# Optimization experiments

Measured on AMD Instinct MI355X. Metric: run time of the kernel, lower is better.

## Reference

```python
import jax, jax.numpy as jnp
import numpy as np

N = 100000   # nodes
F = 32       # input features
E = 1600000  # edges
G = 512      # graphs
EPS = 1e-5   # BatchNorm eps


def setup_inputs() -> dict:
    key = jax.random.key(0)
    ks = jax.random.split(key, 12)
    x = jax.random.normal(ks[0], (N, F), jnp.float32)
    edge_index = jax.random.randint(ks[1], (2, E), 0, N)
    batch = jnp.sort(jax.random.randint(ks[2], (N,), 0, G))

    def glorot(k, i, o):
        return jax.random.normal(k, (i, o), jnp.float32) * (1.0 / np.sqrt(i))

    return {
        "x": x, "edge_index": edge_index, "batch": batch,
        "W1": glorot(ks[3], F, 16), "b1": jnp.zeros((16,), jnp.float32),
        "g1": jnp.ones((16,), jnp.float32), "be1": jnp.zeros((16,), jnp.float32),
        "W2": glorot(ks[4], 16, 64), "b2": jnp.zeros((64,), jnp.float32),
        "g2": jnp.ones((64,), jnp.float32), "be2": jnp.zeros((64,), jnp.float32),
        "W3": glorot(ks[5], 64, 64), "b3": jnp.zeros((64,), jnp.float32),
        "Wc": glorot(ks[6], 64, 1), "bc": jnp.zeros((1,), jnp.float32),
    }


def _gcn_conv(h, src, dst, dis, W, b, n):
    # PyG GCNConv: D^{-1/2}(A+I)D^{-1/2} X W + b (self-loops folded in analytically)
    hw = h @ W                                   # [N, out]
    msg = hw[src] * (dis[src] * dis[dst])[:, None]   # gather + normalize, [E, out]
    agg = jax.ops.segment_sum(msg, dst, num_segments=n)  # scatter-add
    agg = agg + hw * (dis * dis)[:, None]        # self-loop contribution
    return agg + b


def _bn(h, g, b):
    # BatchNorm1d, training mode (biased variance over node axis)
    m = jnp.mean(h, axis=0)
    v = jnp.mean((h - m) ** 2, axis=0)
    return (h - m) * jax.lax.rsqrt(v + EPS) * g + b


def reference(x, edge_index, batch, W1, b1, g1, be1, W2, b2, g2, be2, W3, b3, Wc, bc):
    n = x.shape[0]
    src, dst = edge_index[0], edge_index[1]
    # degree including self-loops (computed on target nodes, edge weight 1)
    deg = jax.ops.segment_sum(jnp.ones((src.shape[0],), x.dtype), dst, num_segments=n) + 1.0
    dis = jax.lax.rsqrt(deg)

    h = jnp.tanh(_gcn_conv(x, src, dst, dis, W1, b1, n))
    h = _bn(h, g1, be1)
    h = jnp.tanh(_gcn_conv(h, src, dst, dis, W2, b2, n))
    h = _bn(h, g2, be2)
    h = jnp.tanh(_gcn_conv(h, src, dst, dis, W3, b3, n))

    # global_mean_pool over graph ids
    sums = jax.ops.segment_sum(h, batch, num_segments=G)          # [G, 64]
    cnts = jax.ops.segment_sum(jnp.ones((n,), x.dtype), batch, num_segments=G)
    pooled = sums / jnp.maximum(cnts, 1.0)[:, None]

    return pooled @ Wc + bc   # [G, 1]
```

## Files before the change

### kernel.cpp

```cpp
#include <hip/hip_runtime.h>

#define EPSV 1e-5f
#define EB 512
#define NPB 256
#define NBUK_MAX 512

typedef __attribute__((ext_vector_type(8))) short bf16x8;
typedef __attribute__((ext_vector_type(4))) float f32x4;
typedef unsigned short ushort_t;

__device__ inline unsigned f2bf(float f){
  unsigned u = __float_as_uint(f);
  u += 0x7fffu + ((u>>16)&1u);
  return u>>16;
}
#define BF_LO(u) __uint_as_float((u)<<16)
#define BF_HI(u) __uint_as_float((u)&0xffff0000u)

__global__ __launch_bounds__(256) void k_csr_count(const int* __restrict__ dst, int E, int chunk,
                                                   int nbuk, int* __restrict__ cnt){
  __shared__ int hist[NBUK_MAX];
  int t = threadIdx.x, b = blockIdx.x;
  for(int k=t; k<nbuk; k+=256) hist[k]=0;
  __syncthreads();
  int lo = b*chunk, hi = lo+chunk < E ? lo+chunk : E;
  for(int i=lo+t*4; i+3<hi; i+=1024){
    int4 d4 = *(const int4*)(dst + i);
    atomicAdd(&hist[d4.x>>8], 1); atomicAdd(&hist[d4.y>>8], 1);
    atomicAdd(&hist[d4.z>>8], 1); atomicAdd(&hist[d4.w>>8], 1);
  }
  int rem = lo + ((hi - lo) & ~3);
  for(int i=rem+t; i<hi; i+=256) atomicAdd(&hist[dst[i]>>8], 1);
  __syncthreads();
  for(int k=t; k<nbuk; k+=256) cnt[(size_t)k*EB + b] = hist[k];
}

__global__ __launch_bounds__(1024) void k_scan_local(const int* __restrict__ v_in, int L,
                                                     int* __restrict__ loc, int* __restrict__ blk){
  __shared__ int ps[1024];
  int t = threadIdx.x;
  int i = blockIdx.x*1024 + t;
  int v = (i < L) ? v_in[i] : 0;
  ps[t] = v;
  __syncthreads();
  for(int off=1; off<1024; off<<=1){
    int u = (t>=off) ? ps[t-off] : 0;
    __syncthreads();
    ps[t] += u;
    __syncthreads();
  }
  if(i < L) loc[i] = ps[t] - v;
  if(t == 1023) blk[blockIdx.x] = ps[t];
}

__global__ __launch_bounds__(1024) void k_scan_sums(int* __restrict__ blk, int nb,
                                                    int* __restrict__ totalOut){
  __shared__ int ps[1024];
  int t = threadIdx.x;
  int v = (t < nb) ? blk[t] : 0;
  ps[t] = v;
  __syncthreads();
  for(int off=1; off<1024; off<<=1){
    int u = (t>=off) ? ps[t-off] : 0;
    __syncthreads();
    ps[t] += u;
    __syncthreads();
  }
  if(t < nb) blk[t] = ps[t] - v;
  if(t == 1023) *totalOut = ps[t];
}

__global__ __launch_bounds__(256) void k_csr_scatter(const int* __restrict__ src,
                                                     const int* __restrict__ dst,
                                                     const int* __restrict__ loc,
                                                     const int* __restrict__ blk,
                                                     int E, int chunk, int nbuk,
                                                     unsigned* __restrict__ epk){
  __shared__ int cur[NBUK_MAX];
  int t = threadIdx.x, b = blockIdx.x;
  for(int k=t; k<nbuk; k+=256){
    int i = k*EB + b;
    cur[k] = loc[i] + blk[i>>10];
  }
  __syncthreads();
  int lo = b*chunk, hi = lo+chunk < E ? lo+chunk : E;
  for(int i=lo+t*4; i+3<hi; i+=1024){
    int4 s4 = *(const int4*)(src + i);
    int4 d4 = *(const int4*)(dst + i);
    int p0 = atomicAdd(&cur[d4.x>>8], 1);
    epk[p0] = ((unsigned)s4.x<<8) | (unsigned)(d4.x & 255);
    int p1 = atomicAdd(&cur[d4.y>>8], 1);
    epk[p1] = ((unsigned)s4.y<<8) | (unsigned)(d4.y & 255);
    int p2 = atomicAdd(&cur[d4.z>>8], 1);
    epk[p2] = ((unsigned)s4.z<<8) | (unsigned)(d4.z & 255);
    int p3 = atomicAdd(&cur[d4.w>>8], 1);
    epk[p3] = ((unsigned)s4.w<<8) | (unsigned)(d4.w & 255);
  }
  int rem = lo + ((hi - lo) & ~3);
  for(int i=rem+t; i<hi; i+=256){
    int d = dst[i];
    int p = atomicAdd(&cur[d>>8], 1);
    epk[p] = ((unsigned)src[i]<<8) | (unsigned)(d & 255);
  }
}

__global__ __launch_bounds__(256) void k_csr_final(const unsigned* __restrict__ epk,
                                                   const int* __restrict__ loc,
                                                   const int* __restrict__ blk,
                                                   int nbuk, int N, int E,
                                                   int* __restrict__ rp, float* __restrict__ dis,
                                                   int* __restrict__ csr_src){
  __shared__ int hist[NPB], ps[NPB], cur[NPB];
  int t = threadIdx.x, k = blockIdx.x;
  int i0 = k*EB;
  int base = loc[i0] + blk[i0>>10];
  int next;
  if(k+1 < nbuk){ int i1 = (k+1)*EB; next = loc[i1] + blk[i1>>10]; }
  else next = E;
  int cntk = next - base;
  int node0 = k*NPB;
  hist[t] = 0;
  __syncthreads();
  for(int i=t; i<cntk; i+=256) atomicAdd(&hist[(int)(epk[base+i] & 255u)], 1);
  __syncthreads();
  int deg = hist[t];
  ps[t] = deg;
  __syncthreads();
  for(int off=1; off<256; off<<=1){
    int u = (t>=off) ? ps[t-off] : 0;
    __syncthreads();
    ps[t] += u;
    __syncthreads();
  }
  int lb = ps[t] - deg;
  int n = node0 + t;
  if(n < N){
    rp[n]  = base + lb;
    dis[n] = rsqrtf((float)deg + 1.0f);
  }
  cur[t] = base + lb;
  __syncthreads();
  for(int i=t; i<cntk; i+=256){
    unsigned e = epk[base+i];
    int p = atomicAdd(&cur[(int)(e & 255u)], 1);
    csr_src[p] = (int)(e >> 8);
  }
  if(k == nbuk-1 && t == 0) rp[N] = E;
}

__global__ __launch_bounds__(256) void k_gemm1(const float* __restrict__ x,
                                               const float* __restrict__ W,
                                               const float* __restrict__ dis,
                                               int N, ushort_t* __restrict__ P1){
  __shared__ __align__(16) float Ws[32*16];
  int t = threadIdx.x;
  for(int i=t; i<32*16; i+=256) Ws[i] = W[i];
  __syncthreads();
  int row = blockIdx.x*256 + t;
  if(row >= N) return;
  const float4* xr = (const float4*)(x + (size_t)row*32);
  float acc[16];
  #pragma unroll
  for(int j=0;j<16;j++) acc[j]=0.f;
  #pragma unroll
  for(int k4=0;k4<8;k4++){
    float4 v = xr[k4];
    float vv[4] = {v.x, v.y, v.z, v.w};
    #pragma unroll
    for(int kk=0;kk<4;kk++){
      float h = vv[kk];
      const float* wr = &Ws[(k4*4+kk)*16];
      #pragma unroll
      for(int j=0;j<16;j++) acc[j] += h*wr[j];
    }
  }
  float d = dis[row];
  unsigned q[8];
  #pragma unroll
  for(int j=0;j<8;j++)
    q[j] = f2bf(acc[2*j]*d) | (f2bf(acc[2*j+1]*d)<<16);
  uint4* o = (uint4*)(P1 + (size_t)row*16);
  o[0] = make_uint4(q[0],q[1],q[2],q[3]);
  o[1] = make_uint4(q[4],q[5],q[6],q[7]);
}

__global__ __launch_bounds__(256) void k_gather1(const int* __restrict__ rp,
    const int* __restrict__ csr_src,
    const float* __restrict__ dis, const ushort_t* __restrict__ P1,
    const float* __restrict__ bias, int N, ushort_t* __restrict__ Q1,
    float* __restrict__ sdis, float* __restrict__ partials){
  int t = threadIdx.x;
  int idx = blockIdx.x*256 + t;
  int n = idx >> 1, g = t & 1;
  float v[8];
  #pragma unroll
  for(int j=0;j<8;j++) v[j]=0.f;

  if(n < N){
    int beg = rp[n], end = rp[n+1];
    const uint4* Pv = (const uint4*)P1;
    uint4 u = Pv[(size_t)n*2 + g];
    float a0 = BF_LO(u.x), a1 = BF_HI(u.x), a2 = BF_LO(u.y), a3 = BF_HI(u.y);
    float a4 = BF_LO(u.z), a5 = BF_HI(u.z), a6 = BF_LO(u.w), a7 = BF_HI(u.w);
    float b0=0.f,b1=0.f,b2=0.f,b3=0.f,b4=0.f,b5=0.f,b6=0.f,b7=0.f;
    float sd = 0.f;
    int j = beg;
    for(; j+3 < end; j += 4){
      int s0 = csr_src[j], s1 = csr_src[j+1], s2 = csr_src[j+2], s3 = csr_src[j+3];
      uint4 u0 = Pv[(size_t)s0*2 + g];
      uint4 u1 = Pv[(size_t)s1*2 + g];
      uint4 u2 = Pv[(size_t)s2*2 + g];
      uint4 u3 = Pv[(size_t)s3*2 + g];
      if(g==0) sd += (dis[s0] + dis[s1]) + (dis[s2] + dis[s3]);
      a0 += BF_LO(u0.x); a1 += BF_HI(u0.x); a2 += BF_LO(u0.y); a3 += BF_HI(u0.y);
      a4 += BF_LO(u0.z); a5 += BF_HI(u0.z); a6 += BF_LO(u0.w); a7 += BF_HI(u0.w);
      b0 += BF_LO(u1.x); b1 += BF_HI(u1.x); b2 += BF_LO(u1.y); b3 += BF_HI(u1.y);
      b4 += BF_LO(u1.z); b5 += BF_HI(u1.z); b6 += BF_LO(u1.w); b7 += BF_HI(u1.w);
      a0 += BF_LO(u2.x); a1 += BF_HI(u2.x); a2 += BF_LO(u2.y); a3 += BF_HI(u2.y);
      a4 += BF_LO(u2.z); a5 += BF_HI(u2.z); a6 += BF_LO(u2.w); a7 += BF_HI(u2.w);
      b0 += BF_LO(u3.x); b1 += BF_HI(u3.x); b2 += BF_LO(u3.y); b3 += BF_HI(u3.y);
      b4 += BF_LO(u3.z); b5 += BF_HI(u3.z); b6 += BF_LO(u3.w); b7 += BF_HI(u3.w);
    }
    for(; j < end; ++j){
      int s0 = csr_src[j];
      uint4 u0 = Pv[(size_t)s0*2 + g];
      if(g==0) sd += dis[s0];
      a0 += BF_LO(u0.x); a1 += BF_HI(u0.x); a2 += BF_LO(u0.y); a3 += BF_HI(u0.y);
      a4 += BF_LO(u0.z); a5 += BF_HI(u0.z); a6 += BF_LO(u0.w); a7 += BF_HI(u0.w);
    }
    float d = dis[n];
    float4 bb0 = *(const float4*)(bias + g*8);
    float4 bb1 = *(const float4*)(bias + g*8 + 4);
    v[0] = tanhf((a0+b0)*d + bb0.x); v[1] = tanhf((a1+b1)*d + bb0.y);
    v[2] = tanhf((a2+b2)*d + bb0.z); v[3] = tanhf((a3+b3)*d + bb0.w);
    v[4] = tanhf((a4+b4)*d + bb1.x); v[5] = tanhf((a5+b5)*d + bb1.y);
    v[6] = tanhf((a6+b6)*d + bb1.z); v[7] = tanhf((a7+b7)*d + bb1.w);
    uint4 o;
    o.x = f2bf(v[0]*d) | (f2bf(v[1]*d)<<16);
    o.y = f2bf(v[2]*d) | (f2bf(v[3]*d)<<16);
    o.z = f2bf(v[4]*d) | (f2bf(v[5]*d)<<16);
    o.w = f2bf(v[6]*d) | (f2bf(v[7]*d)<<16);
    *(uint4*)(Q1 + (size_t)n*16 + g*8) = o;
    if(g==0) sdis[n] = sd;
  }

  int lane = t & 63, wid = t >> 6;
  __shared__ float redS[4][2][8], redQ[4][2][8];
  #pragma unroll
  for(int j=0;j<8;j++){
    float s = v[j], q = v[j]*v[j];
    #pragma unroll
    for(int off=32; off>=2; off>>=1){
      s += __shfl_down(s, off, 64);
      q += __shfl_down(q, off, 64);
    }
    if(lane < 2){ redS[wid][lane][j] = s; redQ[wid][lane][j] = q; }
  }
  __syncthreads();
  if(t < 16){
    int gg = t>>3, j = t&7;
    float S = redS[0][gg][j]+redS[1][gg][j]+redS[2][gg][j]+redS[3][gg][j];
    float Q = redQ[0][gg][j]+redQ[1][gg][j]+redQ[2][gg][j]+redQ[3][gg][j];
    partials[(size_t)blockIdx.x*32 + t]      = S;
    partials[(size_t)blockIdx.x*32 + 16 + t] = Q;
  }
}

template<int C>
__global__ __launch_bounds__(256) void k_bn_red(const float* __restrict__ partials, int nblk,
                                                float* __restrict__ red){
  constexpr int W = 2*C;
  constexpr int RPF = 256/W;
  int t = threadIdx.x;
  int c = t % W, r0 = t / W;
  float acc = 0.f;
  for(int r = blockIdx.x*RPF + r0; r < nblk; r += 64*RPF)
    acc += partials[(size_t)r*W + c];
  __shared__ float ls[256];
  ls[t] = acc;
  __syncthreads();
  if(t < W){
    float s = 0.f;
    #pragma unroll
    for(int k=0;k<RPF;k++) s += ls[k*W + t];
    red[blockIdx.x*W + t] = s;
  }
}

__global__ __launch_bounds__(256) void k_bn_finprep2b(const float* __restrict__ red,
                           const float* __restrict__ gw, const float* __restrict__ be,
                           float invN, const float* __restrict__ W,
                           ushort_t* __restrict__ wf, float* __restrict__ cp){
  __shared__ float s0[16], s1[16], scf[16], shf[16];
  int t = threadIdx.x;
  if(t < 32){
    float s = 0.f;
    for(int r=0;r<64;r++) s += red[r*32 + t];
    if(t < 16) s0[t] = s; else s1[t-16] = s;
  }
  __syncthreads();
  if(t < 16){
    float m = s0[t]*invN;
    float var = fmaxf(s1[t]*invN - m*m, 0.f);
    float inv = rsqrtf(var + EPSV);
    float sc = gw[t]*inv;
    scf[t] = sc;
    shf[t] = be[t] - m*sc;
  }
  __syncthreads();
  int total = 4*64*8;
  for(int idx=t; idx<total; idx+=256){
    int e = idx & 7;
    int l = (idx>>3) & 63;
    int ct = idx>>9;
    int k = (l>>4)*8 + e;
    int col = ct*16 + (l&15);
    float v = (k < 16) ? scf[k]*W[k*64 + col] : 0.f;
    wf[idx] = (ushort_t)f2bf(v);
  }
  if(t < 64){
    float s = 0.f;
    for(int k=0;k<16;k++) s += shf[k]*W[k*64 + t];
    cp[t] = s;
  }
}

__global__ __launch_bounds__(256) void k_bn_finprep3(const float* __restrict__ red,
                           const float* __restrict__ gw, const float* __restrict__ be,
                           float invN, const float* __restrict__ W,
                           ushort_t* __restrict__ wf, float* __restrict__ cp){
  __shared__ float s0[64], s1[64], scf[64], shf[64];
  int t = threadIdx.x;
  if(t < 128){
    float s = 0.f;
    for(int r=0;r<64;r++) s += red[r*128 + t];
    if(t < 64) s0[t] = s; else s1[t-64] = s;
  }
  __syncthreads();
  if(t < 64){
    float m = s0[t]*invN;
    float var = fmaxf(s1[t]*invN - m*m, 0.f);
    float inv = rsqrtf(var + EPSV);
    float sc = gw[t]*inv;
    scf[t] = sc;
    shf[t] = be[t] - m*sc;
  }
  __syncthreads();
  int total = 4*2*64*8;
  for(int idx=t; idx<total; idx+=256){
    int e = idx & 7;
    int l = (idx>>3) & 63;
    int slot = idx>>9;
    int ct = slot>>1, half = slot&1;
    int k = (l>>4)*8 + e + half*32;
    int col = ct*16 + (l&15);
    wf[idx] = (ushort_t)f2bf(scf[k]*W[k*64 + col]);
  }
  if(t < 64){
    float s = 0.f;
    for(int k=0;k<64;k++) s += shf[k]*W[k*64 + t];
    cp[t] = s;
  }
}

__global__ __launch_bounds__(256) void k_gather2(const int* __restrict__ rp,
    const int* __restrict__ csr_src, const ushort_t* __restrict__ Q1,
    int N, ushort_t* __restrict__ M2){
  int t = threadIdx.x;
  int idx = blockIdx.x*256 + t;
  int n = idx >> 1, g = t & 1;
  if(n >= N) return;
  int beg = rp[n], end = rp[n+1];
  const uint4* Pv = (const uint4*)Q1;
  uint4 u = Pv[(size_t)n*2 + g];
  float a0 = BF_LO(u.x), a1 = BF_HI(u.x), a2 = BF_LO(u.y), a3 = BF_HI(u.y);
  float a4 = BF_LO(u.z), a5 = BF_HI(u.z), a6 = BF_LO(u.w), a7 = BF_HI(u.w);
  float b0=0.f,b1=0.f,b2=0.f,b3=0.f,b4=0.f,b5=0.f,b6=0.f,b7=0.f;
  int j = beg;
  for(; j+3 < end; j += 4){
    int s0 = csr_src[j], s1 = csr_src[j+1], s2 = csr_src[j+2], s3 = csr_src[j+3];
    uint4 u0 = Pv[(size_t)s0*2 + g];
    uint4 u1 = Pv[(size_t)s1*2 + g];
    uint4 u2 = Pv[(size_t)s2*2 + g];
    uint4 u3 = Pv[(size_t)s3*2 + g];
    a0 += BF_LO(u0.x); a1 += BF_HI(u0.x); a2 += BF_LO(u0.y); a3 += BF_HI(u0.y);
    a4 += BF_LO(u0.z); a5 += BF_HI(u0.z); a6 += BF_LO(u0.w); a7 += BF_HI(u0.w);
    b0 += BF_LO(u1.x); b1 += BF_HI(u1.x); b2 += BF_LO(u1.y); b3 += BF_HI(u1.y);
    b4 += BF_LO(u1.z); b5 += BF_HI(u1.z); b6 += BF_LO(u1.w); b7 += BF_HI(u1.w);
    a0 += BF_LO(u2.x); a1 += BF_HI(u2.x); a2 += BF_LO(u2.y); a3 += BF_HI(u2.y);
    a4 += BF_LO(u2.z); a5 += BF_HI(u2.z); a6 += BF_LO(u2.w); a7 += BF_HI(u2.w);
    b0 += BF_LO(u3.x); b1 += BF_HI(u3.x); b2 += BF_LO(u3.y); b3 += BF_HI(u3.y);
    b4 += BF_LO(u3.z); b5 += BF_HI(u3.z); b6 += BF_LO(u3.w); b7 += BF_HI(u3.w);
  }
  for(; j < end; ++j){
    int s0 = csr_src[j];
    uint4 u0 = Pv[(size_t)s0*2 + g];
    a0 += BF_LO(u0.x); a1 += BF_HI(u0.x); a2 += BF_LO(u0.y); a3 += BF_HI(u0.y);
    a4 += BF_LO(u0.z); a5 += BF_HI(u0.z); a6 += BF_LO(u0.w); a7 += BF_HI(u0.w);
  }
  uint4 o;
  o.x = f2bf(a0+b0) | (f2bf(a1+b1)<<16);
  o.y = f2bf(a2+b2) | (f2bf(a3+b3)<<16);
  o.z = f2bf(a4+b4) | (f2bf(a5+b5)<<16);
  o.w = f2bf(a6+b6) | (f2bf(a7+b7)<<16);
  *(uint4*)(M2 + (size_t)n*16 + g*8) = o;
}

__global__ __launch_bounds__(256) void k_mfma2(const ushort_t* __restrict__ M2,
                                               const ushort_t* __restrict__ wf,
                                               const float* __restrict__ cp,
                                               const float* __restrict__ dis,
                                               const float* __restrict__ sdis,
                                               const float* __restrict__ b2,
                                               int N, ushort_t* __restrict__ Q2,
                                               float* __restrict__ partials){
  int t = threadIdx.x, wid = t>>6, l = t&63;
  int r0 = blockIdx.x*128 + wid*32;

  bf16x8 bfr[4];
  #pragma unroll
  for(int ct=0; ct<4; ct++)
    bfr[ct] = *(const bf16x8*)(wf + ((size_t)ct*64 + l)*8);

  bf16x8 af[2];
  #pragma unroll
  for(int rt=0; rt<2; rt++){
    int arow = r0 + rt*16 + (l&15);
    int k0 = (l>>4)*8;
    if(arow < N && k0 < 16) af[rt] = *(const bf16x8*)(M2 + (size_t)arow*16 + k0);
    else                    af[rt] = (bf16x8){0,0,0,0,0,0,0,0};
  }

  f32x4 acc[2][4];
  #pragma unroll
  for(int rt=0; rt<2; rt++)
    #pragma unroll
    for(int ct=0; ct<4; ct++)
      acc[rt][ct] = (f32x4){0.f,0.f,0.f,0.f};

  #pragma unroll
  for(int rt=0; rt<2; rt++)
    #pragma unroll
    for(int ct=0; ct<4; ct++)
      acc[rt][ct] = __builtin_amdgcn_mfma_f32_16x16x32_bf16(af[rt], bfr[ct], acc[rt][ct], 0, 0, 0);

  float cpc[4], blc[4];
  #pragma unroll
  for(int ct=0; ct<4; ct++){
    int col = ct*16 + (l&15);
    cpc[ct] = cp[col]; blc[ct] = b2[col];
  }

  float S4[4] = {0.f,0.f,0.f,0.f}, Q4[4] = {0.f,0.f,0.f,0.f};
  #pragma unroll
  for(int rt=0; rt<2; rt++){
    int rbase = r0 + rt*16 + (l>>4)*4;
    #pragma unroll
    for(int reg=0; reg<4; reg++){
      int row = rbase + reg;
      if(row < N){
        float d = dis[row];
        float sg = sdis[row] + d;
        #pragma unroll
        for(int ct=0; ct<4; ct++){
          float h = tanhf(d*(acc[rt][ct][reg] + sg*cpc[ct]) + blc[ct]);
          Q2[(size_t)row*64 + ct*16 + (l&15)] = (ushort_t)f2bf(h*d);
          S4[ct] += h; Q4[ct] += h*h;
        }
      }
    }
  }
  #pragma unroll
  for(int ct=0; ct<4; ct++){
    S4[ct] += __shfl_xor(S4[ct], 16, 64);
    S4[ct] += __shfl_xor(S4[ct], 32, 64);
    Q4[ct] += __shfl_xor(Q4[ct], 16, 64);
    Q4[ct] += __shfl_xor(Q4[ct], 32, 64);
  }
  __shared__ float wsm[4][64], wqm[4][64];
  if(l < 16){
    #pragma unroll
    for(int ct=0; ct<4; ct++){
      wsm[wid][ct*16 + l] = S4[ct];
      wqm[wid][ct*16 + l] = Q4[ct];
    }
  }
  __syncthreads();
  if(t < 64){
    float S = wsm[0][t]+wsm[1][t]+wsm[2][t]+wsm[3][t];
    float Q = wqm[0][t]+wqm[1][t]+wqm[2][t]+wqm[3][t];
    partials[(size_t)blockIdx.x*128 + t]      = S;
    partials[(size_t)blockIdx.x*128 + 64 + t] = Q;
  }
}

__global__ __launch_bounds__(256) void k_gather3(const int* __restrict__ rp,
    const int* __restrict__ csr_src, const ushort_t* __restrict__ Q2,
    int N, ushort_t* __restrict__ M3){
  int t = threadIdx.x;
  int idx = blockIdx.x*256 + t;
  int n = idx >> 3, g = t & 7;
  if(n >= N) return;
  int beg = rp[n], end = rp[n+1];
  const uint4* Pv = (const uint4*)Q2;
  uint4 u = Pv[(size_t)n*8 + g];
  float a0 = BF_LO(u.x), a1 = BF_HI(u.x), a2 = BF_LO(u.y), a3 = BF_HI(u.y);
  float a4 = BF_LO(u.z), a5 = BF_HI(u.z), a6 = BF_LO(u.w), a7 = BF_HI(u.w);
  float b0=0.f,b1=0.f,b2=0.f,b3=0.f,b4=0.f,b5=0.f,b6=0.f,b7=0.f;
  int j = beg;
  for(; j+3 < end; j += 4){
    int s0 = csr_src[j], s1 = csr_src[j+1], s2 = csr_src[j+2], s3 = csr_src[j+3];
    uint4 u0 = Pv[(size_t)s0*8 + g];
    uint4 u1 = Pv[(size_t)s1*8 + g];
    uint4 u2 = Pv[(size_t)s2*8 + g];
    uint4 u3 = Pv[(size_t)s3*8 + g];
    a0 += BF_LO(u0.x); a1 += BF_HI(u0.x); a2 += BF_LO(u0.y); a3 += BF_HI(u0.y);
    a4 += BF_LO(u0.z); a5 += BF_HI(u0.z); a6 += BF_LO(u0.w); a7 += BF_HI(u0.w);
    b0 += BF_LO(u1.x); b1 += BF_HI(u1.x); b2 += BF_LO(u1.y); b3 += BF_HI(u1.y);
    b4 += BF_LO(u1.z); b5 += BF_HI(u1.z); b6 += BF_LO(u1.w); b7 += BF_HI(u1.w);
    a0 += BF_LO(u2.x); a1 += BF_HI(u2.x); a2 += BF_LO(u2.y); a3 += BF_HI(u2.y);
    a4 += BF_LO(u2.z); a5 += BF_HI(u2.z); a6 += BF_LO(u2.w); a7 += BF_HI(u2.w);
    b0 += BF_LO(u3.x); b1 += BF_HI(u3.x); b2 += BF_LO(u3.y); b3 += BF_HI(u3.y);
    b4 += BF_LO(u3.z); b5 += BF_HI(u3.z); b6 += BF_LO(u3.w); b7 += BF_HI(u3.w);
  }
  for(; j < end; ++j){
    int s0 = csr_src[j];
    uint4 u0 = Pv[(size_t)s0*8 + g];
    a0 += BF_LO(u0.x); a1 += BF_HI(u0.x); a2 += BF_LO(u0.y); a3 += BF_HI(u0.y);
    a4 += BF_LO(u0.z); a5 += BF_HI(u0.z); a6 += BF_LO(u0.w); a7 += BF_HI(u0.w);
  }
  uint4 o;
  o.x = f2bf(a0+b0) | (f2bf(a1+b1)<<16);
  o.y = f2bf(a2+b2) | (f2bf(a3+b3)<<16);
  o.z = f2bf(a4+b4) | (f2bf(a5+b5)<<16);
  o.w = f2bf(a6+b6) | (f2bf(a7+b7)<<16);
  *(uint4*)(M3 + (size_t)n*8*8 + g*8) = o;
}

__global__ __launch_bounds__(256) void k_mfma_head(const ushort_t* __restrict__ M3,
                                                   const ushort_t* __restrict__ wf,
                                                   const float* __restrict__ cp,
                                                   const float* __restrict__ dis,
                                                   const float* __restrict__ sdis,
                                                   const float* __restrict__ b3,
                                                   const float* __restrict__ Wc,
                                                   int N, float* __restrict__ y){
  int t = threadIdx.x, wid = t>>6, l = t&63;
  int r0 = blockIdx.x*128 + wid*32;

  bf16x8 bfr[4][2];
  #pragma unroll
  for(int ct=0; ct<4; ct++)
    #pragma unroll
    for(int h=0; h<2; h++)
      bfr[ct][h] = *(const bf16x8*)(wf + ((size_t)(ct*2+h)*64 + l)*8);

  bf16x8 af[2][2];
  #pragma unroll
  for(int rt=0; rt<2; rt++){
    int arow = r0 + rt*16 + (l&15);
    int k0 = (l>>4)*8;
    #pragma unroll
    for(int h=0; h<2; h++){
      if(arow < N) af[rt][h] = *(const bf16x8*)(M3 + (size_t)arow*64 + k0 + h*32);
      else         af[rt][h] = (bf16x8){0,0,0,0,0,0,0,0};
    }
  }

  f32x4 acc[2][4];
  #pragma unroll
  for(int rt=0; rt<2; rt++)
    #pragma unroll
    for(int ct=0; ct<4; ct++)
      acc[rt][ct] = (f32x4){0.f,0.f,0.f,0.f};

  #pragma unroll
  for(int rt=0; rt<2; rt++)
    #pragma unroll
    for(int ct=0; ct<4; ct++)
      #pragma unroll
      for(int h=0; h<2; h++)
        acc[rt][ct] = __builtin_amdgcn_mfma_f32_16x16x32_bf16(af[rt][h], bfr[ct][h], acc[rt][ct], 0, 0, 0);

  float cpc[4], blc[4], wcc[4];
  #pragma unroll
  for(int ct=0; ct<4; ct++){
    int col = ct*16 + (l&15);
    cpc[ct] = cp[col]; blc[ct] = b3[col]; wcc[ct] = Wc[col];
  }

  #pragma unroll
  for(int rt=0; rt<2; rt++){
    int rbase = r0 + rt*16 + (l>>4)*4;
    #pragma unroll
    for(int reg=0; reg<4; reg++){
      int row = rbase + reg;
      bool ok = (row < N);
      float d  = ok ? dis[row] : 0.f;
      float sg = ok ? (sdis[row] + d) : 0.f;
      float s = 0.f;
      #pragma unroll
      for(int ct=0; ct<4; ct++){
        float h = tanhf(d*(acc[rt][ct][reg] + sg*cpc[ct]) + blc[ct]);
        s += h*wcc[ct];
      }
      s += __shfl_xor(s, 1, 64);
      s += __shfl_xor(s, 2, 64);
      s += __shfl_xor(s, 4, 64);
      s += __shfl_xor(s, 8, 64);
      if(ok && (l&15)==0) y[row] = s;
    }
  }
}

__global__ __launch_bounds__(64) void k_pool2(const float* __restrict__ y,
                                              const int* __restrict__ batch, int N,
                                              const float* __restrict__ bc,
                                              float* __restrict__ out){
  int gId = blockIdx.x;
  int t = threadIdx.x;
  int lo=0, hi=N;
  while(lo<hi){ int mid=(lo+hi)>>1; if(batch[mid] < gId) lo=mid+1; else hi=mid; }
  int start = lo;
  lo=start; hi=N;
  while(lo<hi){ int mid=(lo+hi)>>1; if(batch[mid] < gId+1) lo=mid+1; else hi=mid; }
  int end = lo;

  float s = 0.f;
  for(int r = start+t; r < end; r += 64) s += y[r];
  #pragma unroll
  for(int o=32; o>0; o>>=1) s += __shfl_down(s, o, 64);
  if(t == 0){
    float cnt = (float)(end - start);
    out[gId] = s / fmaxf(cnt, 1.0f) + bc[0];
  }
}

extern "C" void kernel_launch(void* const* d_in, const int* in_sizes, int n_in,
                              void* d_out, int out_size, void* d_ws, size_t ws_size,
                              hipStream_t stream) {
  const float* x     = (const float*)d_in[0];
  const int*   ei    = (const int*)d_in[1];
  const int*   batch = (const int*)d_in[2];
  const float* W1 = (const float*)d_in[3];
  const float* b1 = (const float*)d_in[4];
  const float* g1 = (const float*)d_in[5];
  const float* be1= (const float*)d_in[6];
  const float* W2 = (const float*)d_in[7];
  const float* b2 = (const float*)d_in[8];
  const float* g2 = (const float*)d_in[9];
  const float* be2= (const float*)d_in[10];
  const float* W3 = (const float*)d_in[11];
  const float* b3 = (const float*)d_in[12];
  const float* Wc = (const float*)d_in[13];
  const float* bc = (const float*)d_in[14];

  int N = in_sizes[2];
  int E = in_sizes[1] / 2;
  int G = out_size;
  const int* srcp = ei;
  const int* dstp = ei + E;
  float* out = (float*)d_out;

  auto cdiv = [](long long a, long long b){ return (int)((a+b-1)/b); };
  auto al16 = [](size_t s){ return (s + 15) & ~(size_t)15; };
  int nbuk  = cdiv(N, NPB);
  int chunk = 4*cdiv(E, (long long)EB*4);
  int L     = nbuk * EB;
  int nbL   = cdiv(L, 1024);
  int nblk16 = cdiv((long long)N*2, 256);
  int nblk64 = cdiv((long long)N*8, 256);
  int nblkM  = cdiv(N, 128);

  char* w = (char*)d_ws;
  ushort_t* Q1       = (ushort_t*)w; w += al16((size_t)N*16*2);
  ushort_t* P1       = (ushort_t*)w; w += al16((size_t)N*16*2);
  ushort_t* M2       = (ushort_t*)w; w += al16((size_t)N*16*2);
  ushort_t* Q2       = (ushort_t*)w; w += al16((size_t)N*64*2);
  ushort_t* M3       = (ushort_t*)w; w += al16((size_t)N*64*2);
  float*    dis      = (float*)w;    w += al16((size_t)N*4);
  float*    sdis     = (float*)w;    w += al16((size_t)N*4);
  float*    yv       = (float*)w;    w += al16((size_t)N*4);
  int*      row_ptr  = (int*)w;      w += al16((size_t)(N+1)*4);
  int*      csr_src  = (int*)w;      w += al16((size_t)E*4);
  unsigned* epk      = (unsigned*)w; w += al16((size_t)E*4);
  int*      cnt      = (int*)w;      w += al16((size_t)L*4);
  int*      scan_loc = (int*)w;      w += al16((size_t)L*4);
  int*      scan_blk = (int*)w;      w += al16(1024*4);
  float*    partials = (float*)w;    w += al16((size_t)nblk64*128*4);
  float*    red      = (float*)w;    w += al16(64*128*4);
  float*    cp       = (float*)w;    w += al16(64*4);
  ushort_t* wf       = (ushort_t*)w; w += al16(8*64*8*2);

  k_csr_count<<<EB,256,0,stream>>>(dstp, E, chunk, nbuk, cnt);
  k_scan_local<<<nbL,1024,0,stream>>>(cnt, L, scan_loc, scan_blk);
  k_scan_sums<<<1,1024,0,stream>>>(scan_blk, nbL, row_ptr + N);
  k_csr_scatter<<<EB,256,0,stream>>>(srcp, dstp, scan_loc, scan_blk, E, chunk, nbuk, epk);
  k_csr_final<<<nbuk,256,0,stream>>>(epk, scan_loc, scan_blk, nbuk, N, E, row_ptr, dis, csr_src);

  k_gemm1<<<cdiv(N,256),256,0,stream>>>(x, W1, dis, N, P1);
  k_gather1<<<nblk16,256,0,stream>>>(row_ptr, csr_src, dis, P1, b1, N, Q1, sdis, partials);
  k_bn_red<16><<<64,256,0,stream>>>(partials, nblk16, red);
  k_bn_finprep2b<<<1,256,0,stream>>>(red, g1, be1, 1.0f/N, W2, wf, cp);

  k_gather2<<<nblk16,256,0,stream>>>(row_ptr, csr_src, Q1, N, M2);
  k_mfma2<<<nblkM,256,0,stream>>>(M2, wf, cp, dis, sdis, b2, N, Q2, partials);
  k_bn_red<64><<<64,256,0,stream>>>(partials, nblkM, red);
  k_bn_finprep3<<<1,256,0,stream>>>(red, g2, be2, 1.0f/N, W3, wf, cp);

  k_gather3<<<nblk64,256,0,stream>>>(row_ptr, csr_src, Q2, N, M3);
  k_mfma_head<<<cdiv(N,128),256,0,stream>>>(M3, wf, cp, dis, sdis, b3, Wc, N, yv);

  k_pool2<<<G,64,0,stream>>>(yv, batch, N, bc, out);
}
```

Measured before the change: 176.4 us.

## Fuse layer-3 neighbor gather into MFMA head kernel, dropping M3 buffer

The third-layer CSR gather is merged with the MFMA matmul/tanh/classifier head. Each lane now gathers 16 features of one row, laid out directly as the MFMA A-fragment, so the bf16 M3 intermediate is never written to or re-read from global memory and one launch is removed. In exchange each thread does twice the gather work (two uint4 loads per neighbor), uses more registers, and the grid shrinks to 64 rows per block. That cuts the number of independent gather threads, which may reduce latency hiding. Partials sizing is adjusted to the remaining block count.

```diff
diff --git a/kernel.cpp b/kernel.cpp
--- a/kernel.cpp
+++ b/kernel.cpp
@@ -494,93 +494,80 @@
   }
 }
 
-__global__ __launch_bounds__(256) void k_gather3(const int* __restrict__ rp,
+__global__ __launch_bounds__(256) void k_g3head(const int* __restrict__ rp,
     const int* __restrict__ csr_src, const ushort_t* __restrict__ Q2,
-    int N, ushort_t* __restrict__ M3){
-  int t = threadIdx.x;
-  int idx = blockIdx.x*256 + t;
-  int n = idx >> 3, g = t & 7;
-  if(n >= N) return;
-  int beg = rp[n], end = rp[n+1];
-  const uint4* Pv = (const uint4*)Q2;
-  uint4 u = Pv[(size_t)n*8 + g];
-  float a0 = BF_LO(u.x), a1 = BF_HI(u.x), a2 = BF_LO(u.y), a3 = BF_HI(u.y);
-  float a4 = BF_LO(u.z), a5 = BF_HI(u.z), a6 = BF_LO(u.w), a7 = BF_HI(u.w);
-  float b0=0.f,b1=0.f,b2=0.f,b3=0.f,b4=0.f,b5=0.f,b6=0.f,b7=0.f;
-  int j = beg;
-  for(; j+3 < end; j += 4){
-    int s0 = csr_src[j], s1 = csr_src[j+1], s2 = csr_src[j+2], s3 = csr_src[j+3];
-    uint4 u0 = Pv[(size_t)s0*8 + g];
-    uint4 u1 = Pv[(size_t)s1*8 + g];
-    uint4 u2 = Pv[(size_t)s2*8 + g];
-    uint4 u3 = Pv[(size_t)s3*8 + g];
-    a0 += BF_LO(u0.x); a1 += BF_HI(u0.x); a2 += BF_LO(u0.y); a3 += BF_HI(u0.y);
-    a4 += BF_LO(u0.z); a5 += BF_HI(u0.z); a6 += BF_LO(u0.w); a7 += BF_HI(u0.w);
-    b0 += BF_LO(u1.x); b1 += BF_HI(u1.x); b2 += BF_LO(u1.y); b3 += BF_HI(u1.y);
-    b4 += BF_LO(u1.z); b5 += BF_HI(u1.z); b6 += BF_LO(u1.w); b7 += BF_HI(u1.w);
-    a0 += BF_LO(u2.x); a1 += BF_HI(u2.x); a2 += BF_LO(u2.y); a3 += BF_HI(u2.y);
-    a4 += BF_LO(u2.z); a5 += BF_HI(u2.z); a6 += BF_LO(u2.w); a7 += BF_HI(u2.w);
-    b0 += BF_LO(u3.x); b1 += BF_HI(u3.x); b2 += BF_LO(u3.y); b3 += BF_HI(u3.y);
-    b4 += BF_LO(u3.z); b5 += BF_HI(u3.z); b6 += BF_LO(u3.w); b7 += BF_HI(u3.w);
-  }
-  for(; j < end; ++j){
-    int s0 = csr_src[j];
-    uint4 u0 = Pv[(size_t)s0*8 + g];
-    a0 += BF_LO(u0.x); a1 += BF_HI(u0.x); a2 += BF_LO(u0.y); a3 += BF_HI(u0.y);
-    a4 += BF_LO(u0.z); a5 += BF_HI(u0.z); a6 += BF_LO(u0.w); a7 += BF_HI(u0.w);
-  }
-  uint4 o;
-  o.x = f2bf(a0+b0) | (f2bf(a1+b1)<<16);
-  o.y = f2bf(a2+b2) | (f2bf(a3+b3)<<16);
-  o.z = f2bf(a4+b4) | (f2bf(a5+b5)<<16);
-  o.w = f2bf(a6+b6) | (f2bf(a7+b7)<<16);
-  *(uint4*)(M3 + (size_t)n*8*8 + g*8) = o;
-}
-
-__global__ __launch_bounds__(256) void k_mfma_head(const ushort_t* __restrict__ M3,
-                                                   const ushort_t* __restrict__ wf,
-                                                   const float* __restrict__ cp,
-                                                   const float* __restrict__ dis,
-                                                   const float* __restrict__ sdis,
-                                                   const float* __restrict__ b3,
-                                                   const float* __restrict__ Wc,
-                                                   int N, float* __restrict__ y){
+    const ushort_t* __restrict__ wf, const float* __restrict__ cp,
+    const float* __restrict__ dis, const float* __restrict__ sdis,
+    const float* __restrict__ b3, const float* __restrict__ Wc,
+    int N, float* __restrict__ y){
   int t = threadIdx.x, wid = t>>6, l = t&63;
-  int r0 = blockIdx.x*128 + wid*32;
-
-  bf16x8 bfr[4][2];
-  #pragma unroll
-  for(int ct=0; ct<4; ct++)
-    #pragma unroll
-    for(int h=0; h<2; h++)
-      bfr[ct][h] = *(const bf16x8*)(wf + ((size_t)(ct*2+h)*64 + l)*8);
-
-  bf16x8 af[2][2];
-  #pragma unroll
-  for(int rt=0; rt<2; rt++){
-    int arow = r0 + rt*16 + (l&15);
-    int k0 = (l>>4)*8;
-    #pragma unroll
-    for(int h=0; h<2; h++){
-      if(arow < N) af[rt][h] = *(const bf16x8*)(M3 + (size_t)arow*64 + k0 + h*32);
-      else         af[rt][h] = (bf16x8){0,0,0,0,0,0,0,0};
-    }
-  }
-
-  f32x4 acc[2][4];
-  #pragma unroll
-  for(int rt=0; rt<2; rt++)
-    #pragma unroll
-    for(int ct=0; ct<4; ct++)
-      acc[rt][ct] = (f32x4){0.f,0.f,0.f,0.f};
-
-  #pragma unroll
-  for(int rt=0; rt<2; rt++)
-    #pragma unroll
-    for(int ct=0; ct<4; ct++)
-      #pragma unroll
-      for(int h=0; h<2; h++)
-        acc[rt][ct] = __builtin_amdgcn_mfma_f32_16x16x32_bf16(af[rt][h], bfr[ct][h], acc[rt][ct], 0, 0, 0);
+  int r0 = blockIdx.x*64 + wid*16;
+  int row = r0 + (l&15);
+  int kc = l>>4;
+  bool ok = (row < N);
+
+  float A[16];
+  #pragma unroll
+  for(int j=0;j<16;j++) A[j]=0.f;
+
+  if(ok){
+    const uint4* Pv = (const uint4*)Q2;
+    int beg = rp[row], end = rp[row+1];
+    uint4 u0 = Pv[(size_t)row*8 + kc];
+    uint4 u1 = Pv[(size_t)row*8 + 4 + kc];
+    A[0]+=BF_LO(u0.x); A[1]+=BF_HI(u0.x); A[2]+=BF_LO(u0.y); A[3]+=BF_HI(u0.y);
+    A[4]+=BF_LO(u0.z); A[5]+=BF_HI(u0.z); A[6]+=BF_LO(u0.w); A[7]+=BF_HI(u0.w);
+    A[8]+=BF_LO(u1.x); A[9]+=BF_HI(u1.x); A[10]+=BF_LO(u1.y); A[11]+=BF_HI(u1.y);
+    A[12]+=BF_LO(u1.z); A[13]+=BF_HI(u1.z); A[14]+=BF_LO(u1.w); A[15]+=BF_HI(u1.w);
+    int j = beg;
+    for(; j+3 < end; j += 4){
+      int s0 = csr_src[j], s1 = csr_src[j+1], s2 = csr_src[j+2], s3 = csr_src[j+3];
+      uint4 v0 = Pv[(size_t)s0*8 + kc],     w0 = Pv[(size_t)s0*8 + 4 + kc];
+      uint4 v1 = Pv[(size_t)s1*8 + kc],     w1 = Pv[(size_t)s1*8 + 4 + kc];
+      uint4 v2 = Pv[(size_t)s2*8 + kc],     w2 = Pv[(size_t)s2*8 + 4 + kc];
+      uint4 v3 = Pv[(size_t)s3*8 + kc],     w3 = Pv[(size_t)s3*8 + 4 + kc];
+      A[0]+=BF_LO(v0.x); A[1]+=BF_HI(v0.x); A[2]+=BF_LO(v0.y); A[3]+=BF_HI(v0.y);
+      A[4]+=BF_LO(v0.z); A[5]+=BF_HI(v0.z); A[6]+=BF_LO(v0.w); A[7]+=BF_HI(v0.w);
+      A[8]+=BF_LO(w0.x); A[9]+=BF_HI(w0.x); A[10]+=BF_LO(w0.y); A[11]+=BF_HI(w0.y);
+      A[12]+=BF_LO(w0.z); A[13]+=BF_HI(w0.z); A[14]+=BF_LO(w0.w); A[15]+=BF_HI(w0.w);
+      A[0]+=BF_LO(v1.x); A[1]+=BF_HI(v1.x); A[2]+=BF_LO(v1.y); A[3]+=BF_HI(v1.y);
+      A[4]+=BF_LO(v1.z); A[5]+=BF_HI(v1.z); A[6]+=BF_LO(v1.w); A[7]+=BF_HI(v1.w);
+      A[8]+=BF_LO(w1.x); A[9]+=BF_HI(w1.x); A[10]+=BF_LO(w1.y); A[11]+=BF_HI(w1.y);
+      A[12]+=BF_LO(w1.z); A[13]+=BF_HI(w1.z); A[14]+=BF_LO(w1.w); A[15]+=BF_HI(w1.w);
+      A[0]+=BF_LO(v2.x); A[1]+=BF_HI(v2.x); A[2]+=BF_LO(v2.y); A[3]+=BF_HI(v2.y);
+      A[4]+=BF_LO(v2.z); A[5]+=BF_HI(v2.z); A[6]+=BF_LO(v2.w); A[7]+=BF_HI(v2.w);
+      A[8]+=BF_LO(w2.x); A[9]+=BF_HI(w2.x); A[10]+=BF_LO(w2.y); A[11]+=BF_HI(w2.y);
+      A[12]+=BF_LO(w2.z); A[13]+=BF_HI(w2.z); A[14]+=BF_LO(w2.w); A[15]+=BF_HI(w2.w);
+      A[0]+=BF_LO(v3.x); A[1]+=BF_HI(v3.x); A[2]+=BF_LO(v3.y); A[3]+=BF_HI(v3.y);
+      A[4]+=BF_LO(v3.z); A[5]+=BF_HI(v3.z); A[6]+=BF_LO(v3.w); A[7]+=BF_HI(v3.w);
+      A[8]+=BF_LO(w3.x); A[9]+=BF_HI(w3.x); A[10]+=BF_LO(w3.y); A[11]+=BF_HI(w3.y);
+      A[12]+=BF_LO(w3.z); A[13]+=BF_HI(w3.z); A[14]+=BF_LO(w3.w); A[15]+=BF_HI(w3.w);
+    }
+    for(; j < end; ++j){
+      int s0 = csr_src[j];
+      uint4 v0 = Pv[(size_t)s0*8 + kc], w0 = Pv[(size_t)s0*8 + 4 + kc];
+      A[0]+=BF_LO(v0.x); A[1]+=BF_HI(v0.x); A[2]+=BF_LO(v0.y); A[3]+=BF_HI(v0.y);
+      A[4]+=BF_LO(v0.z); A[5]+=BF_HI(v0.z); A[6]+=BF_LO(v0.w); A[7]+=BF_HI(v0.w);
+      A[8]+=BF_LO(w0.x); A[9]+=BF_HI(w0.x); A[10]+=BF_LO(w0.y); A[11]+=BF_HI(w0.y);
+      A[12]+=BF_LO(w0.z); A[13]+=BF_HI(w0.z); A[14]+=BF_LO(w0.w); A[15]+=BF_HI(w0.w);
+    }
+  }
+
+  bf16x8 af0, af1;
+  af0[0]=(short)f2bf(A[0]); af0[1]=(short)f2bf(A[1]); af0[2]=(short)f2bf(A[2]); af0[3]=(short)f2bf(A[3]);
+  af0[4]=(short)f2bf(A[4]); af0[5]=(short)f2bf(A[5]); af0[6]=(short)f2bf(A[6]); af0[7]=(short)f2bf(A[7]);
+  af1[0]=(short)f2bf(A[8]); af1[1]=(short)f2bf(A[9]); af1[2]=(short)f2bf(A[10]); af1[3]=(short)f2bf(A[11]);
+  af1[4]=(short)f2bf(A[12]); af1[5]=(short)f2bf(A[13]); af1[6]=(short)f2bf(A[14]); af1[7]=(short)f2bf(A[15]);
+
+  f32x4 acc[4];
+  #pragma unroll
+  for(int ct=0; ct<4; ct++){
+    bf16x8 b0 = *(const bf16x8*)(wf + ((size_t)(ct*2+0)*64 + l)*8);
+    bf16x8 b1 = *(const bf16x8*)(wf + ((size_t)(ct*2+1)*64 + l)*8);
+    acc[ct] = (f32x4){0.f,0.f,0.f,0.f};
+    acc[ct] = __builtin_amdgcn_mfma_f32_16x16x32_bf16(af0, b0, acc[ct], 0, 0, 0);
+    acc[ct] = __builtin_amdgcn_mfma_f32_16x16x32_bf16(af1, b1, acc[ct], 0, 0, 0);
+  }
 
   float cpc[4], blc[4], wcc[4];
   #pragma unroll
@@ -589,27 +576,24 @@
     cpc[ct] = cp[col]; blc[ct] = b3[col]; wcc[ct] = Wc[col];
   }
 
-  #pragma unroll
-  for(int rt=0; rt<2; rt++){
-    int rbase = r0 + rt*16 + (l>>4)*4;
-    #pragma unroll
-    for(int reg=0; reg<4; reg++){
-      int row = rbase + reg;
-      bool ok = (row < N);
-      float d  = ok ? dis[row] : 0.f;
-      float sg = ok ? (sdis[row] + d) : 0.f;
-      float s = 0.f;
-      #pragma unroll
-      for(int ct=0; ct<4; ct++){
-        float h = tanhf(d*(acc[rt][ct][reg] + sg*cpc[ct]) + blc[ct]);
-        s += h*wcc[ct];
-      }
-      s += __shfl_xor(s, 1, 64);
-      s += __shfl_xor(s, 2, 64);
-      s += __shfl_xor(s, 4, 64);
-      s += __shfl_xor(s, 8, 64);
-      if(ok && (l&15)==0) y[row] = s;
-    }
+  int rbase = r0 + (l>>4)*4;
+  #pragma unroll
+  for(int reg=0; reg<4; reg++){
+    int rowo = rbase + reg;
+    bool ok2 = (rowo < N);
+    float d  = ok2 ? dis[rowo] : 0.f;
+    float sg = ok2 ? (sdis[rowo] + d) : 0.f;
+    float s = 0.f;
+    #pragma unroll
+    for(int ct=0; ct<4; ct++){
+      float h = tanhf(d*(acc[ct][reg] + sg*cpc[ct]) + blc[ct]);
+      s += h*wcc[ct];
+    }
+    s += __shfl_xor(s, 1, 64);
+    s += __shfl_xor(s, 2, 64);
+    s += __shfl_xor(s, 4, 64);
+    s += __shfl_xor(s, 8, 64);
+    if(ok2 && (l&15)==0) y[rowo] = s;
   }
 }
 
@@ -669,7 +653,6 @@
   int L     = nbuk * EB;
   int nbL   = cdiv(L, 1024);
   int nblk16 = cdiv((long long)N*2, 256);
-  int nblk64 = cdiv((long long)N*8, 256);
   int nblkM  = cdiv(N, 128);
 
   char* w = (char*)d_ws;
@@ -677,7 +660,6 @@
   ushort_t* P1       = (ushort_t*)w; w += al16((size_t)N*16*2);
   ushort_t* M2       = (ushort_t*)w; w += al16((size_t)N*16*2);
   ushort_t* Q2       = (ushort_t*)w; w += al16((size_t)N*64*2);
-  ushort_t* M3       = (ushort_t*)w; w += al16((size_t)N*64*2);
   float*    dis      = (float*)w;    w += al16((size_t)N*4);
   float*    sdis     = (float*)w;    w += al16((size_t)N*4);
   float*    yv       = (float*)w;    w += al16((size_t)N*4);
@@ -687,7 +669,7 @@
   int*      cnt      = (int*)w;      w += al16((size_t)L*4);
   int*      scan_loc = (int*)w;      w += al16((size_t)L*4);
   int*      scan_blk = (int*)w;      w += al16(1024*4);
-  float*    partials = (float*)w;    w += al16((size_t)nblk64*128*4);
+  float*    partials = (float*)w;    w += al16((size_t)nblkM*128*4);
   float*    red      = (float*)w;    w += al16(64*128*4);
   float*    cp       = (float*)w;    w += al16(64*4);
   ushort_t* wf       = (ushort_t*)w; w += al16(8*64*8*2);
@@ -708,8 +690,7 @@
   k_bn_red<64><<<64,256,0,stream>>>(partials, nblkM, red);
   k_bn_finprep3<<<1,256,0,stream>>>(red, g2, be2, 1.0f/N, W3, wf, cp);
 
-  k_gather3<<<nblk64,256,0,stream>>>(row_ptr, csr_src, Q2, N, M3);
-  k_mfma_head<<<cdiv(N,128),256,0,stream>>>(M3, wf, cp, dis, sdis, b3, Wc, N, yv);
+  k_g3head<<<cdiv(N,64),256,0,stream>>>(row_ptr, csr_src, Q2, wf, cp, dis, sdis, b3, Wc, N, yv);
 
   k_pool2<<<G,64,0,stream>>>(yv, batch, N, bc, out);
 }
```

New measurement: 179.3 us. No clear change (+1.7%).
